# Kernel tuning notes

Hardware: AMD Instinct MI355X
Metric: run time of the kernel (lower is better)

Reference implementation:

```python
import jax, jax.numpy as jnp
import numpy as np

NUM_FEATURES = 1_000_000
EMB_DIM = 16
NUM_FIELDS = 39
CIN_SIZES = (200, 200, 200)
DNN_SIZES = (400, 400)


def setup_inputs() -> dict:
    key = jax.random.key(0)
    ks = jax.random.split(key, 16)
    B = 2048
    inp = {}
    inp["feature_ids"] = jax.random.randint(ks[0], (B, NUM_FIELDS), 0, NUM_FEATURES)
    inp["feature_vals"] = jax.random.uniform(ks[1], (B, NUM_FIELDS), dtype=jnp.float32)
    # embeddings (xavier-normal-ish scale)
    inp["emb"] = jax.random.normal(ks[2], (NUM_FEATURES, EMB_DIM), jnp.float32) * 0.02
    inp["bias_emb"] = jax.random.normal(ks[3], (NUM_FEATURES, 1), jnp.float32) * 0.02
    # CIN conv1d (kernel size 1) weights: (out, in)
    field_nums = [NUM_FIELDS]
    for i, size in enumerate(CIN_SIZES):
        cin_in = field_nums[-1] * NUM_FIELDS
        inp[f"cin_W{i}"] = jax.random.normal(ks[4 + i], (size, cin_in), jnp.float32) / np.sqrt(cin_in)
        inp[f"cin_b{i}"] = jnp.zeros((size,), jnp.float32)
        field_nums.append(size // 2 if i != len(CIN_SIZES) - 1 else size)
    # DNN linears: (out, in)
    last = NUM_FIELDS * EMB_DIM
    for i, size in enumerate(DNN_SIZES):
        inp[f"dnn_W{i}"] = jax.random.normal(ks[8 + i], (size, last), jnp.float32) / np.sqrt(last)
        inp[f"dnn_b{i}"] = jnp.zeros((size,), jnp.float32)
        last = size
    hidden_size = sum(CIN_SIZES[:-1]) // 2 + CIN_SIZES[-1]  # 400
    fc_in = hidden_size + DNN_SIZES[-1]
    inp["fc_W"] = jax.random.normal(ks[12], (1, fc_in), jnp.float32) / np.sqrt(fc_in)
    inp["fc_b"] = jnp.zeros((1,), jnp.float32)
    return inp


def _forward(feature_ids, feature_vals, emb, bias_emb,
             cin_W0, cin_b0, cin_W1, cin_b1, cin_W2, cin_b2,
             dnn_W0, dnn_b0, dnn_W1, dnn_b1, fc_W, fc_b):
    B = feature_ids.shape[0]
    inputs = emb[feature_ids] * feature_vals[:, :, None]        # [B, F, D]
    input_biases = bias_emb[feature_ids][..., 0] * feature_vals  # [B, F]

    # CIN
    Ws = (cin_W0, cin_W1, cin_W2)
    bs = (cin_b0, cin_b1, cin_b2)
    h = inputs
    finals = []
    n_layers = len(CIN_SIZES)
    for i in range(n_layers):
        size = CIN_SIZES[i]
        x = jnp.einsum('bhd,bmd->bhmd', h, inputs)              # [B, H, F, D]
        x = x.reshape(B, -1, EMB_DIM)                           # [B, H*F, D]
        x = jnp.einsum('bcd,oc->bod', x, Ws[i]) + bs[i][None, :, None]  # 1x1 conv
        x = jax.nn.relu(x)
        if i != n_layers - 1:
            h, direct = x[:, : size // 2], x[:, size // 2:]
        else:
            direct = x
        finals.append(direct)
    cin_result = jnp.sum(jnp.concatenate(finals, axis=1), axis=-1)  # [B, hidden]

    # DNN
    d = inputs.reshape(B, -1)
    d = jax.nn.relu(d @ dnn_W0.T + dnn_b0)
    d = jax.nn.relu(d @ dnn_W1.T + dnn_b1)

    out = (jnp.concatenate((cin_result, d), axis=1) @ fc_W.T + fc_b)[:, 0]
    return out + jnp.sum(input_biases, axis=1)                  # [B]


def reference(feature_ids, feature_vals, emb, bias_emb,
              cin_W0, cin_b0, cin_W1, cin_b1, cin_W2, cin_b2,
              dnn_W0, dnn_b0, dnn_W1, dnn_b1, fc_W, fc_b):
    return _forward(feature_ids, feature_vals, emb, bias_emb,
                    cin_W0, cin_b0, cin_W1, cin_b1, cin_W2, cin_b2,
                    dnn_W0, dnn_b0, dnn_W1, dnn_b1, fc_W, fc_b)
```

## Files before the change

kernel.cpp:

```cpp
#include <hip/hip_runtime.h>

#define B 2048
#define NF 39
#define D 16

typedef __bf16 bf16x8 __attribute__((ext_vector_type(8)));
typedef float f32x4 __attribute__((ext_vector_type(4)));

__global__ __launch_bounds__(256) void gather_kernel(
    const int* __restrict__ fid, const float* __restrict__ fval,
    const float* __restrict__ emb, const float* __restrict__ bias_emb,
    float* __restrict__ inputs, float* __restrict__ biassum) {
  int b = blockIdx.x;
  __shared__ int ids[NF];
  __shared__ float vals[NF];
  int t = threadIdx.x;
  if (t < NF) { ids[t] = fid[b * NF + t]; vals[t] = fval[b * NF + t]; }
  __syncthreads();
  for (int i = t; i < NF * D; i += 256) {
    int f = i >> 4, d = i & 15;
    inputs[b * NF * D + i] = emb[(long)ids[f] * D + d] * vals[f];
  }
  if (t < 64) {
    float pb = (t < NF) ? bias_emb[ids[t]] * vals[t] : 0.f;
#pragma unroll
    for (int m = 32; m >= 1; m >>= 1) pb += __shfl_xor(pb, m);
    if (t == 0) biassum[b] = pb;
  }
}

__global__ void prep_w_kernel(const float* __restrict__ W, __bf16* __restrict__ Wg,
                              int Hreal, int nch) {
  int idx = blockIdx.x * 256 + threadIdx.x;
  int total = nch * 13 * 64;
  if (idx >= total) return;
  int l = idx & 63;
  int mt = (idx >> 6) % 13;
  int c = idx / (13 * 64);
  int o = mt * 16 + (l & 15);
  int kb = c * 32 + ((l >> 4) << 3);
  int rowlen = Hreal * 39;
  bf16x8 v;
#pragma unroll
  for (int j = 0; j < 8; ++j) {
    int k = kb + j;
    int h = k / 40;
    int m = k - h * 40;
    float val = 0.f;
    if (o < 200 && h < Hreal && m < 39) val = W[(long)o * rowlen + h * 39 + m];
    v[j] = (__bf16)val;
  }
  *reinterpret_cast<bf16x8*>(Wg + (long)idx * 8) = v;
}

__global__ void prep_dnn_w(const float* __restrict__ W, __bf16* __restrict__ Wd,
                           int IN, int nch) {
  int idx = blockIdx.x * 256 + threadIdx.x;
  int total = nch * 25 * 64;
  if (idx >= total) return;
  int l = idx & 63;
  int tt = (idx >> 6) % 25;
  int c = idx / (25 * 64);
  int o = tt * 16 + (l & 15);
  int kb = c * 32 + ((l >> 4) << 3);
  bf16x8 v;
#pragma unroll
  for (int j = 0; j < 8; ++j) {
    int k = kb + j;
    v[j] = (k < IN) ? (__bf16)W[(long)o * IN + k] : (__bf16)0.f;
  }
  *reinterpret_cast<bf16x8*>(Wd + (long)idx * 8) = v;
}

__device__ __forceinline__ void form_x(const float* Hs, const float* Zs,
                                       __bf16* xbuf, int k0, int col) {
  int h = (int)((unsigned)k0 / 40u);
  int m0 = k0 - h * 40;
  float hv = Hs[h * 64 + col];
  const float4* zp = reinterpret_cast<const float4*>(Zs + col * 44 + m0);
  float4 za = zp[0], zb = zp[1];
  bf16x8 xv;
  xv[0] = (__bf16)(hv * za.x); xv[1] = (__bf16)(hv * za.y);
  xv[2] = (__bf16)(hv * za.z); xv[3] = (__bf16)(hv * za.w);
  xv[4] = (__bf16)(hv * zb.x); xv[5] = (__bf16)(hv * zb.y);
  xv[6] = (__bf16)(hv * zb.z); xv[7] = (__bf16)(hv * zb.w);
  int g = (k0 >> 3) & 7;
  *reinterpret_cast<bf16x8*>(
      reinterpret_cast<char*>(xbuf) + col * 128 + ((g * 16) ^ ((col & 7) << 4))) = xv;
}

template <int W, int NST, int SPLIT>
__device__ __forceinline__ void cin_core3(
    const float* Hs, const float* Zs, __bf16* Xs,
    const __bf16* __restrict__ Wg, const float* __restrict__ bias,
    float* __restrict__ h_next, float* __restrict__ cin_out,
    int col_offset, int bbase, int t) {
  constexpr int TLO = (13 * W) >> 2;
  const int l = t & 63;
  const int q = l >> 4;
  const int dd = l & 15;
  const int colw = t & 63;
  const __bf16* wl = Wg + l * 8;

  f32x4 acc[13] = {};
  bf16x8 wf[8], wfn[8];
#pragma unroll
  for (int i = 0; i < 4; ++i)
#pragma unroll
    for (int hf = 0; hf < 2; ++hf)
      wf[i * 2 + hf] =
          *reinterpret_cast<const bf16x8*>(wl + (long)((hf * 13 + TLO + i) * 64) * 8);

  form_x(Hs, Zs, Xs, (W) * 8, colw);
  form_x(Hs, Zs, Xs, (W + 4) * 8, colw);
  __syncthreads();

  for (int s = 0; s < NST; ++s) {
    __bf16* xcur = Xs + (s & 1) * (64 * 64);
    __bf16* xnxt = Xs + ((s + 1) & 1) * (64 * 64);
    if (s + 1 < NST) {
#pragma unroll
      for (int i = 0; i < 4; ++i)
#pragma unroll
        for (int hf = 0; hf < 2; ++hf)
          wfn[i * 2 + hf] = *reinterpret_cast<const bf16x8*>(
              wl + (long)((((s + 1) * 2 + hf) * 13 + TLO + i) * 64) * 8);
      form_x(Hs, Zs, xnxt, (s + 1) * 64 + W * 8, colw);
      form_x(Hs, Zs, xnxt, (s + 1) * 64 + (W + 4) * 8, colw);
    }
    bf16x8 bfr[4][2];
#pragma unroll
    for (int f = 0; f < 4; ++f)
#pragma unroll
      for (int hf = 0; hf < 2; ++hf) {
        int col = f * 16 + dd;
        int g = q + hf * 4;
        bfr[f][hf] = *reinterpret_cast<const bf16x8*>(
            reinterpret_cast<const char*>(xcur) + col * 128 +
            ((g * 16) ^ ((col & 7) << 4)));
      }
#pragma unroll
    for (int i = 0; i < 13; ++i) {
      const int p = 13 * W + i;
      const int ti = (p >> 2) - TLO;
      const int f = p & 3;
      acc[i] = __builtin_amdgcn_mfma_f32_16x16x32_bf16(wf[ti * 2 + 0], bfr[f][0],
                                                       acc[i], 0, 0, 0);
      acc[i] = __builtin_amdgcn_mfma_f32_16x16x32_bf16(wf[ti * 2 + 1], bfr[f][1],
                                                       acc[i], 0, 0, 0);
    }
    __syncthreads();
    if (s + 1 < NST) {
#pragma unroll
      for (int i = 0; i < 8; ++i) wf[i] = wfn[i];
    }
  }

#pragma unroll
  for (int i = 0; i < 13; ++i) {
    const int p = 13 * W + i;
    const int tt = p >> 2, f = p & 3;
    const int b = bbase + f;
#pragma unroll
    for (int r = 0; r < 4; ++r) {
      int o = tt * 16 + q * 4 + r;
      if (o < 200) {
        float x = fmaxf(acc[i][r] + bias[o], 0.f);
        if (SPLIT && o < 100) {
          h_next[((long)b * 100 + o) * 16 + dd] = x;
        } else {
          x += __shfl_xor(x, 1);
          x += __shfl_xor(x, 2);
          x += __shfl_xor(x, 4);
          x += __shfl_xor(x, 8);
          if (dd == 0) cin_out[b * 400 + col_offset + o - (SPLIT ? 100 : 0)] = x;
        }
      }
    }
  }
}

template <int HR, int NST, int SPLIT>
__global__ __launch_bounds__(256, 2) void cin_mfma3(
    const float* __restrict__ Zin, const float* __restrict__ Hin,
    const __bf16* __restrict__ Wg, const float* __restrict__ bias,
    float* __restrict__ h_next, float* __restrict__ cin_out, int col_offset) {
  constexpr int HPAD = (NST * 64 + 39) / 40;
  __shared__ float Hs[HPAD * 64];
  __shared__ float Zs[64 * 44];
  __shared__ __bf16 Xs[2 * 64 * 64];
  const int t = threadIdx.x;
  const int bbase = blockIdx.x * 4;

  for (int i = t; i < HPAD * 64; i += 256) {
    int h = i >> 6, col = i & 63;
    int b = bbase + (col >> 4), d = col & 15;
    Hs[i] = (h < HR) ? Hin[((long)b * HR + h) * 16 + d] : 0.f;
  }
  for (int i = t; i < 64 * 40; i += 256) {
    int col = i / 40, m = i - (i / 40) * 40;
    int b = bbase + (col >> 4), d = col & 15;
    Zs[col * 44 + m] = (m < NF) ? Zin[((long)b * NF + m) * 16 + d] : 0.f;
  }
  __syncthreads();

  const int w = t >> 6;
  if (w == 0)
    cin_core3<0, NST, SPLIT>(Hs, Zs, Xs, Wg, bias, h_next, cin_out, col_offset, bbase, t);
  else if (w == 1)
    cin_core3<1, NST, SPLIT>(Hs, Zs, Xs, Wg, bias, h_next, cin_out, col_offset, bbase, t);
  else if (w == 2)
    cin_core3<2, NST, SPLIT>(Hs, Zs, Xs, Wg, bias, h_next, cin_out, col_offset, bbase, t);
  else
    cin_core3<3, NST, SPLIT>(Hs, Zs, Xs, Wg, bias, h_next, cin_out, col_offset, bbase, t);
}

template <int IN>
__device__ __forceinline__ void dnn_stage(const float* __restrict__ x,
                                          __bf16* Xs, int bg, int c, int t) {
  int b = t >> 2, kb = t & 3;
  int k0 = c * 32 + kb * 8;
  bf16x8 v;
  if (k0 < IN) {
    const float4* p = reinterpret_cast<const float4*>(x + (long)(bg * 64 + b) * IN + k0);
    float4 a = p[0], bq = p[1];
    v[0] = (__bf16)a.x;  v[1] = (__bf16)a.y;  v[2] = (__bf16)a.z;  v[3] = (__bf16)a.w;
    v[4] = (__bf16)bq.x; v[5] = (__bf16)bq.y; v[6] = (__bf16)bq.z; v[7] = (__bf16)bq.w;
  } else {
#pragma unroll
    for (int j = 0; j < 8; ++j) v[j] = (__bf16)0.f;
  }
  *reinterpret_cast<bf16x8*>(Xs + ((kb * 64 + b) << 3)) = v;
}

template <int W, int MH, int IN, int NCH>
__device__ __forceinline__ void dnn_core(
    const float* __restrict__ x, const __bf16* __restrict__ Wd,
    const float* __restrict__ bias, float* __restrict__ out,
    __bf16* Xs, int bg, int t) {
  constexpr int NP = MH ? 12 : 13;
  constexpr int TLO = MH ? (13 + 3 * W) : ((13 * W) >> 2);
  constexpr int TN = MH ? 3 : 4;
  constexpr int WLO = MH ? (3 * W) : ((13 * W) >> 2);
  const int l = t & 63;
  const int q = l >> 4, dd = l & 15;
  const __bf16* wl = Wd + l * 8;

  f32x4 acc[NP] = {};
  bf16x8 wf[TN], wfn[TN];
#pragma unroll
  for (int i = 0; i < TN; ++i)
    wf[i] = *reinterpret_cast<const bf16x8*>(wl + (long)((TLO + i) * 64) * 8);

  dnn_stage<IN>(x, Xs, bg, 0, t);
  __syncthreads();

  for (int c = 0; c < NCH; ++c) {
    __bf16* cur = Xs + (c & 1) * 2048;
    __bf16* nxt = Xs + ((c + 1) & 1) * 2048;
    const bool more = (c + 1 < NCH);
    if (more) {
      dnn_stage<IN>(x, nxt, bg, c + 1, t);
#pragma unroll
      for (int i = 0; i < TN; ++i)
        wfn[i] = *reinterpret_cast<const bf16x8*>(
            wl + (long)(((c + 1) * 25 + TLO + i) * 64) * 8);
    }
    bf16x8 bfr[4];
#pragma unroll
    for (int f = 0; f < 4; ++f)
      bfr[f] = *reinterpret_cast<const bf16x8*>(cur + ((q * 64 + f * 16 + dd) << 3));
#pragma unroll
    for (int i = 0; i < NP; ++i) {
      const int p = NP * W + i;
      const int wfi = (p >> 2) - WLO;
      acc[i] = __builtin_amdgcn_mfma_f32_16x16x32_bf16(wf[wfi], bfr[p & 3], acc[i], 0, 0, 0);
    }
    __syncthreads();
    if (more) {
#pragma unroll
      for (int i = 0; i < TN; ++i) wf[i] = wfn[i];
    }
  }

#pragma unroll
  for (int i = 0; i < NP; ++i) {
    const int p = NP * W + i;
    const int gt = (MH ? 13 : 0) + (p >> 2);
    const int f = p & 3;
    const int b = bg * 64 + f * 16 + dd;
#pragma unroll
    for (int r = 0; r < 4; ++r) {
      int o = gt * 16 + q * 4 + r;
      out[(long)b * 400 + o] = fmaxf(acc[i][r] + bias[o], 0.f);
    }
  }
}

template <int IN, int NCH>
__global__ __launch_bounds__(256) void dnn_mfma(
    const float* __restrict__ x, const __bf16* __restrict__ Wd,
    const float* __restrict__ bias, float* __restrict__ out) {
  __shared__ __bf16 Xs[2 * 4 * 64 * 8];
  const int blk = blockIdx.x;
  const int bg = blk >> 1, mh = blk & 1;
  const int t = threadIdx.x;
  const int w = t >> 6;
  if (mh == 0) {
    if (w == 0) dnn_core<0, 0, IN, NCH>(x, Wd, bias, out, Xs, bg, t);
    else if (w == 1) dnn_core<1, 0, IN, NCH>(x, Wd, bias, out, Xs, bg, t);
    else if (w == 2) dnn_core<2, 0, IN, NCH>(x, Wd, bias, out, Xs, bg, t);
    else dnn_core<3, 0, IN, NCH>(x, Wd, bias, out, Xs, bg, t);
  } else {
    if (w == 0) dnn_core<0, 1, IN, NCH>(x, Wd, bias, out, Xs, bg, t);
    else if (w == 1) dnn_core<1, 1, IN, NCH>(x, Wd, bias, out, Xs, bg, t);
    else if (w == 2) dnn_core<2, 1, IN, NCH>(x, Wd, bias, out, Xs, bg, t);
    else dnn_core<3, 1, IN, NCH>(x, Wd, bias, out, Xs, bg, t);
  }
}

__global__ __launch_bounds__(256) void final_kernel(
    const float* __restrict__ cin, const float* __restrict__ d1,
    const float* __restrict__ fcW, const float* __restrict__ fcb,
    const float* __restrict__ biassum, float* __restrict__ out) {
  int b = blockIdx.x, t = threadIdx.x;
  float p = 0.f;
  for (int i = t; i < 800; i += 256) {
    float v = (i < 400) ? cin[b * 400 + i] : d1[b * 400 + (i - 400)];
    p += v * fcW[i];
  }
#pragma unroll
  for (int m = 32; m >= 1; m >>= 1) p += __shfl_xor(p, m);
  __shared__ float red[4];
  if ((t & 63) == 0) red[t >> 6] = p;
  __syncthreads();
  if (t == 0) out[b] = red[0] + red[1] + red[2] + red[3] + fcb[0] + biassum[b];
}

extern "C" void kernel_launch(void* const* d_in, const int* in_sizes, int n_in,
                              void* d_out, int out_size, void* d_ws,
                              size_t ws_size, hipStream_t stream) {
  (void)in_sizes; (void)n_in; (void)out_size; (void)ws_size;
  const int* fid = (const int*)d_in[0];
  const float* fval = (const float*)d_in[1];
  const float* emb = (const float*)d_in[2];
  const float* bias_emb = (const float*)d_in[3];
  const float* cW0 = (const float*)d_in[4];
  const float* cb0 = (const float*)d_in[5];
  const float* cW1 = (const float*)d_in[6];
  const float* cb1 = (const float*)d_in[7];
  const float* cW2 = (const float*)d_in[8];
  const float* cb2 = (const float*)d_in[9];
  const float* dW0 = (const float*)d_in[10];
  const float* db0 = (const float*)d_in[11];
  const float* dW1 = (const float*)d_in[12];
  const float* db1 = (const float*)d_in[13];
  const float* fcW = (const float*)d_in[14];
  const float* fcb = (const float*)d_in[15];
  float* out = (float*)d_out;

  float* ws = (float*)d_ws;
  float* inputs = ws;  ws += B * NF * D;
  float* biassum = ws; ws += B;
  float* h1 = ws;      ws += B * 100 * D;
  float* h2 = ws;      ws += B * 100 * D;
  float* cinres = ws;  ws += B * 400;
  float* dd0 = ws;     ws += B * 400;
  float* dd1 = ws;     ws += B * 400;
  __bf16* Wg0 = (__bf16*)ws; ws += (50 * 13 * 64 * 8) / 2;
  __bf16* Wg1 = (__bf16*)ws; ws += (126 * 13 * 64 * 8) / 2;
  __bf16* Wg2 = (__bf16*)ws; ws += (126 * 13 * 64 * 8) / 2;
  __bf16* Wd0 = (__bf16*)ws; ws += (20 * 25 * 64 * 8) / 2;
  __bf16* Wd1 = (__bf16*)ws; ws += (13 * 25 * 64 * 8) / 2;

  gather_kernel<<<B, 256, 0, stream>>>(fid, fval, emb, bias_emb, inputs, biassum);

  prep_w_kernel<<<(50 * 13 * 64 + 255) / 256, 256, 0, stream>>>(cW0, Wg0, 39, 50);
  prep_w_kernel<<<(126 * 13 * 64 + 255) / 256, 256, 0, stream>>>(cW1, Wg1, 100, 126);
  prep_w_kernel<<<(126 * 13 * 64 + 255) / 256, 256, 0, stream>>>(cW2, Wg2, 100, 126);
  prep_dnn_w<<<(20 * 25 * 64 + 255) / 256, 256, 0, stream>>>(dW0, Wd0, 624, 20);
  prep_dnn_w<<<(13 * 25 * 64 + 255) / 256, 256, 0, stream>>>(dW1, Wd1, 400, 13);

  cin_mfma3<39, 25, 1><<<B / 4, 256, 0, stream>>>(inputs, inputs, Wg0, cb0, h1, cinres, 0);
  cin_mfma3<100, 63, 1><<<B / 4, 256, 0, stream>>>(inputs, h1, Wg1, cb1, h2, cinres, 100);
  cin_mfma3<100, 63, 0><<<B / 4, 256, 0, stream>>>(inputs, h2, Wg2, cb2, nullptr, cinres, 200);

  dnn_mfma<624, 20><<<64, 256, 0, stream>>>(inputs, Wd0, db0, dd0);
  dnn_mfma<400, 13><<<64, 256, 0, stream>>>(dd0, Wd1, db1, dd1);

  final_kernel<<<B, 256, 0, stream>>>(cinres, dd1, fcW, fcb, biassum, out);
}
```

Baseline: 242.7 us.

## Fuse three CIN layers into one kernel and split DNN across more blocks

Merges the three CIN layer kernels into a single kernel that keeps the hidden state H in shared memory between layers. This removes the global round-trips for h1/h2 and two kernel launches. The DNN kernels now split output tiles four ways across 128 blocks instead of two ways across 64, and their staging loads are separated from the LDS writes so global latency overlaps the MFMAs. Both paths use s_setprio around the MFMA loops and a lighter LDS barrier; the fused CIN kernel's larger shared footprint and register use may reduce occupancy.

```diff
diff --git a/kernel.cpp b/kernel.cpp
--- a/kernel.cpp
+++ b/kernel.cpp
@@ -6,6 +6,11 @@
 
 typedef __bf16 bf16x8 __attribute__((ext_vector_type(8)));
 typedef float f32x4 __attribute__((ext_vector_type(4)));
+
+__device__ __forceinline__ void lds_barrier() {
+  asm volatile("s_waitcnt lgkmcnt(0)" ::: "memory");
+  __builtin_amdgcn_s_barrier();
+}
 
 __global__ __launch_bounds__(256) void gather_kernel(
     const int* __restrict__ fid, const float* __restrict__ fval,
@@ -89,44 +94,40 @@
       reinterpret_cast<char*>(xbuf) + col * 128 + ((g * 16) ^ ((col & 7) << 4))) = xv;
 }
 
-template <int W, int NST, int SPLIT>
-__device__ __forceinline__ void cin_core3(
-    const float* Hs, const float* Zs, __bf16* Xs,
+template <int NW, int NST, int SPLIT>
+__device__ __forceinline__ void cin_layer(
+    float* Hs, const float* Zs, __bf16* Xs,
     const __bf16* __restrict__ Wg, const float* __restrict__ bias,
-    float* __restrict__ h_next, float* __restrict__ cin_out,
-    int col_offset, int bbase, int t) {
-  constexpr int TLO = (13 * W) >> 2;
+    float* __restrict__ cin_out, int col_offset, int bbase, int t) {
+  constexpr int TLO = (13 * NW) >> 2;
   const int l = t & 63;
-  const int q = l >> 4;
-  const int dd = l & 15;
-  const int colw = t & 63;
-  const __bf16* wl = Wg + l * 8;
+  const int q = l >> 4, dd = l & 15;
 
   f32x4 acc[13] = {};
   bf16x8 wf[8], wfn[8];
+  const __bf16* wp = Wg + l * 8 + TLO * 512;
 #pragma unroll
   for (int i = 0; i < 4; ++i)
 #pragma unroll
     for (int hf = 0; hf < 2; ++hf)
-      wf[i * 2 + hf] =
-          *reinterpret_cast<const bf16x8*>(wl + (long)((hf * 13 + TLO + i) * 64) * 8);
-
-  form_x(Hs, Zs, Xs, (W) * 8, colw);
-  form_x(Hs, Zs, Xs, (W + 4) * 8, colw);
-  __syncthreads();
+      wf[i * 2 + hf] = *reinterpret_cast<const bf16x8*>(wp + hf * 6656 + i * 512);
+
+  form_x(Hs, Zs, Xs, NW * 8, l);
+  form_x(Hs, Zs, Xs, (NW + 4) * 8, l);
+  lds_barrier();
 
   for (int s = 0; s < NST; ++s) {
-    __bf16* xcur = Xs + (s & 1) * (64 * 64);
-    __bf16* xnxt = Xs + ((s + 1) & 1) * (64 * 64);
-    if (s + 1 < NST) {
+    __bf16* xcur = Xs + (s & 1) * 4096;
+    __bf16* xnxt = Xs + ((s + 1) & 1) * 4096;
+    const bool more = (s + 1 < NST);
+    if (more) {
+      const __bf16* wq = wp + 13312;
 #pragma unroll
       for (int i = 0; i < 4; ++i)
 #pragma unroll
         for (int hf = 0; hf < 2; ++hf)
-          wfn[i * 2 + hf] = *reinterpret_cast<const bf16x8*>(
-              wl + (long)((((s + 1) * 2 + hf) * 13 + TLO + i) * 64) * 8);
-      form_x(Hs, Zs, xnxt, (s + 1) * 64 + W * 8, colw);
-      form_x(Hs, Zs, xnxt, (s + 1) * 64 + (W + 4) * 8, colw);
+          wfn[i * 2 + hf] =
+              *reinterpret_cast<const bf16x8*>(wq + hf * 6656 + i * 512);
     }
     bf16x8 bfr[4][2];
 #pragma unroll
@@ -139,9 +140,14 @@
             reinterpret_cast<const char*>(xcur) + col * 128 +
             ((g * 16) ^ ((col & 7) << 4)));
       }
+    if (more) {
+      form_x(Hs, Zs, xnxt, (s + 1) * 64 + NW * 8, l);
+      form_x(Hs, Zs, xnxt, (s + 1) * 64 + (NW + 4) * 8, l);
+    }
+    __builtin_amdgcn_s_setprio(1);
 #pragma unroll
     for (int i = 0; i < 13; ++i) {
-      const int p = 13 * W + i;
+      const int p = 13 * NW + i;
       const int ti = (p >> 2) - TLO;
       const int f = p & 3;
       acc[i] = __builtin_amdgcn_mfma_f32_16x16x32_bf16(wf[ti * 2 + 0], bfr[f][0],
@@ -149,16 +155,18 @@
       acc[i] = __builtin_amdgcn_mfma_f32_16x16x32_bf16(wf[ti * 2 + 1], bfr[f][1],
                                                        acc[i], 0, 0, 0);
     }
-    __syncthreads();
-    if (s + 1 < NST) {
+    __builtin_amdgcn_s_setprio(0);
+    lds_barrier();
+    if (more) {
 #pragma unroll
       for (int i = 0; i < 8; ++i) wf[i] = wfn[i];
+      wp += 13312;
     }
   }
 
 #pragma unroll
   for (int i = 0; i < 13; ++i) {
-    const int p = 13 * W + i;
+    const int p = 13 * NW + i;
     const int tt = p >> 2, f = p & 3;
     const int b = bbase + f;
 #pragma unroll
@@ -167,7 +175,7 @@
       if (o < 200) {
         float x = fmaxf(acc[i][r] + bias[o], 0.f);
         if (SPLIT && o < 100) {
-          h_next[((long)b * 100 + o) * 16 + dd] = x;
+          Hs[o * 64 + f * 16 + dd] = x;
         } else {
           x += __shfl_xor(x, 1);
           x += __shfl_xor(x, 2);
@@ -178,105 +186,126 @@
       }
     }
   }
-}
-
-template <int HR, int NST, int SPLIT>
-__global__ __launch_bounds__(256, 2) void cin_mfma3(
-    const float* __restrict__ Zin, const float* __restrict__ Hin,
-    const __bf16* __restrict__ Wg, const float* __restrict__ bias,
-    float* __restrict__ h_next, float* __restrict__ cin_out, int col_offset) {
-  constexpr int HPAD = (NST * 64 + 39) / 40;
-  __shared__ float Hs[HPAD * 64];
+  lds_barrier();
+}
+
+template <int NW>
+__device__ __forceinline__ void cin_all(
+    float* Hs, const float* Zs, __bf16* Xs, const __bf16* Wg0,
+    const __bf16* Wg1, const __bf16* Wg2, const float* cb0, const float* cb1,
+    const float* cb2, float* cinres, int bbase, int t) {
+  cin_layer<NW, 25, 1>(Hs, Zs, Xs, Wg0, cb0, cinres, 0, bbase, t);
+  cin_layer<NW, 63, 1>(Hs, Zs, Xs, Wg1, cb1, cinres, 100, bbase, t);
+  cin_layer<NW, 63, 0>(Hs, Zs, Xs, Wg2, cb2, cinres, 200, bbase, t);
+}
+
+__global__ __launch_bounds__(256, 2) void cin_fused(
+    const float* __restrict__ Zin, const __bf16* __restrict__ Wg0,
+    const __bf16* __restrict__ Wg1, const __bf16* __restrict__ Wg2,
+    const float* __restrict__ cb0, const float* __restrict__ cb1,
+    const float* __restrict__ cb2, float* __restrict__ cinres) {
+  __shared__ float Hs[101 * 64];
   __shared__ float Zs[64 * 44];
   __shared__ __bf16 Xs[2 * 64 * 64];
   const int t = threadIdx.x;
   const int bbase = blockIdx.x * 4;
 
-  for (int i = t; i < HPAD * 64; i += 256) {
-    int h = i >> 6, col = i & 63;
-    int b = bbase + (col >> 4), d = col & 15;
-    Hs[i] = (h < HR) ? Hin[((long)b * HR + h) * 16 + d] : 0.f;
-  }
   for (int i = t; i < 64 * 40; i += 256) {
     int col = i / 40, m = i - (i / 40) * 40;
     int b = bbase + (col >> 4), d = col & 15;
     Zs[col * 44 + m] = (m < NF) ? Zin[((long)b * NF + m) * 16 + d] : 0.f;
   }
+  for (int i = t; i < 41 * 64; i += 256) {
+    int h = i >> 6, col = i & 63;
+    int b = bbase + (col >> 4), d = col & 15;
+    Hs[i] = (h < NF) ? Zin[((long)b * NF + h) * 16 + d] : 0.f;
+  }
+  if (t < 64) Hs[100 * 64 + t] = 0.f;
   __syncthreads();
 
   const int w = t >> 6;
-  if (w == 0)
-    cin_core3<0, NST, SPLIT>(Hs, Zs, Xs, Wg, bias, h_next, cin_out, col_offset, bbase, t);
-  else if (w == 1)
-    cin_core3<1, NST, SPLIT>(Hs, Zs, Xs, Wg, bias, h_next, cin_out, col_offset, bbase, t);
-  else if (w == 2)
-    cin_core3<2, NST, SPLIT>(Hs, Zs, Xs, Wg, bias, h_next, cin_out, col_offset, bbase, t);
-  else
-    cin_core3<3, NST, SPLIT>(Hs, Zs, Xs, Wg, bias, h_next, cin_out, col_offset, bbase, t);
+  if (w == 0) cin_all<0>(Hs, Zs, Xs, Wg0, Wg1, Wg2, cb0, cb1, cb2, cinres, bbase, t);
+  else if (w == 1) cin_all<1>(Hs, Zs, Xs, Wg0, Wg1, Wg2, cb0, cb1, cb2, cinres, bbase, t);
+  else if (w == 2) cin_all<2>(Hs, Zs, Xs, Wg0, Wg1, Wg2, cb0, cb1, cb2, cinres, bbase, t);
+  else cin_all<3>(Hs, Zs, Xs, Wg0, Wg1, Wg2, cb0, cb1, cb2, cinres, bbase, t);
 }
 
 template <int IN>
-__device__ __forceinline__ void dnn_stage(const float* __restrict__ x,
-                                          __bf16* Xs, int bg, int c, int t) {
+__device__ __forceinline__ void dnn_stage_load(const float* __restrict__ x,
+                                               int bg, int c, int t,
+                                               float4& a, float4& b2) {
   int b = t >> 2, kb = t & 3;
   int k0 = c * 32 + kb * 8;
+  if (k0 < IN) {
+    const float4* p =
+        reinterpret_cast<const float4*>(x + (long)(bg * 64 + b) * IN + k0);
+    a = p[0];
+    b2 = p[1];
+  } else {
+    a = make_float4(0.f, 0.f, 0.f, 0.f);
+    b2 = make_float4(0.f, 0.f, 0.f, 0.f);
+  }
+}
+
+__device__ __forceinline__ void dnn_stage_write(__bf16* Xs, int t, float4 a,
+                                                float4 b2) {
+  int b = t >> 2, kb = t & 3;
   bf16x8 v;
-  if (k0 < IN) {
-    const float4* p = reinterpret_cast<const float4*>(x + (long)(bg * 64 + b) * IN + k0);
-    float4 a = p[0], bq = p[1];
-    v[0] = (__bf16)a.x;  v[1] = (__bf16)a.y;  v[2] = (__bf16)a.z;  v[3] = (__bf16)a.w;
-    v[4] = (__bf16)bq.x; v[5] = (__bf16)bq.y; v[6] = (__bf16)bq.z; v[7] = (__bf16)bq.w;
-  } else {
-#pragma unroll
-    for (int j = 0; j < 8; ++j) v[j] = (__bf16)0.f;
-  }
+  v[0] = (__bf16)a.x;  v[1] = (__bf16)a.y;  v[2] = (__bf16)a.z;  v[3] = (__bf16)a.w;
+  v[4] = (__bf16)b2.x; v[5] = (__bf16)b2.y; v[6] = (__bf16)b2.z; v[7] = (__bf16)b2.w;
   *reinterpret_cast<bf16x8*>(Xs + ((kb * 64 + b) << 3)) = v;
 }
 
-template <int W, int MH, int IN, int NCH>
+template <int W, int TG, int IN, int NCH>
 __device__ __forceinline__ void dnn_core(
     const float* __restrict__ x, const __bf16* __restrict__ Wd,
-    const float* __restrict__ bias, float* __restrict__ out,
-    __bf16* Xs, int bg, int t) {
-  constexpr int NP = MH ? 12 : 13;
-  constexpr int TLO = MH ? (13 + 3 * W) : ((13 * W) >> 2);
-  constexpr int TN = MH ? 3 : 4;
-  constexpr int WLO = MH ? (3 * W) : ((13 * W) >> 2);
+    const float* __restrict__ bias, float* __restrict__ out, __bf16* Xs,
+    int bg, int t) {
+  constexpr int NT = (TG == 3) ? 7 : 6;
+  constexpr int TGB = TG * 6;
+  constexpr int PLO = NT * W;
+  constexpr int TLO = PLO >> 2;
+  constexpr int TN = ((PLO + NT - 1) >> 2) - TLO + 1;
   const int l = t & 63;
   const int q = l >> 4, dd = l & 15;
   const __bf16* wl = Wd + l * 8;
 
-  f32x4 acc[NP] = {};
+  f32x4 acc[NT] = {};
   bf16x8 wf[TN], wfn[TN];
 #pragma unroll
   for (int i = 0; i < TN; ++i)
-    wf[i] = *reinterpret_cast<const bf16x8*>(wl + (long)((TLO + i) * 64) * 8);
-
-  dnn_stage<IN>(x, Xs, bg, 0, t);
-  __syncthreads();
+    wf[i] = *reinterpret_cast<const bf16x8*>(wl + (long)((TGB + TLO + i) * 64) * 8);
+
+  float4 ra, rb;
+  dnn_stage_load<IN>(x, bg, 0, t, ra, rb);
+  dnn_stage_write(Xs, t, ra, rb);
+  lds_barrier();
 
   for (int c = 0; c < NCH; ++c) {
     __bf16* cur = Xs + (c & 1) * 2048;
     __bf16* nxt = Xs + ((c + 1) & 1) * 2048;
     const bool more = (c + 1 < NCH);
     if (more) {
-      dnn_stage<IN>(x, nxt, bg, c + 1, t);
+      dnn_stage_load<IN>(x, bg, c + 1, t, ra, rb);
 #pragma unroll
       for (int i = 0; i < TN; ++i)
         wfn[i] = *reinterpret_cast<const bf16x8*>(
-            wl + (long)(((c + 1) * 25 + TLO + i) * 64) * 8);
+            wl + (long)(((c + 1) * 25 + TGB + TLO + i) * 64) * 8);
     }
     bf16x8 bfr[4];
 #pragma unroll
     for (int f = 0; f < 4; ++f)
       bfr[f] = *reinterpret_cast<const bf16x8*>(cur + ((q * 64 + f * 16 + dd) << 3));
-#pragma unroll
-    for (int i = 0; i < NP; ++i) {
-      const int p = NP * W + i;
-      const int wfi = (p >> 2) - WLO;
-      acc[i] = __builtin_amdgcn_mfma_f32_16x16x32_bf16(wf[wfi], bfr[p & 3], acc[i], 0, 0, 0);
-    }
-    __syncthreads();
+    __builtin_amdgcn_s_setprio(1);
+#pragma unroll
+    for (int i = 0; i < NT; ++i) {
+      const int p = PLO + i;
+      acc[i] = __builtin_amdgcn_mfma_f32_16x16x32_bf16(wf[(p >> 2) - TLO],
+                                                       bfr[p & 3], acc[i], 0, 0, 0);
+    }
+    __builtin_amdgcn_s_setprio(0);
+    if (more) dnn_stage_write(nxt, t, ra, rb);
+    lds_barrier();
     if (more) {
 #pragma unroll
       for (int i = 0; i < TN; ++i) wf[i] = wfn[i];
@@ -284,9 +313,9 @@
   }
 
 #pragma unroll
-  for (int i = 0; i < NP; ++i) {
-    const int p = NP * W + i;
-    const int gt = (MH ? 13 : 0) + (p >> 2);
+  for (int i = 0; i < NT; ++i) {
+    const int p = PLO + i;
+    const int gt = TGB + (p >> 2);
     const int f = p & 3;
     const int b = bg * 64 + f * 16 + dd;
 #pragma unroll
@@ -303,20 +332,19 @@
     const float* __restrict__ bias, float* __restrict__ out) {
   __shared__ __bf16 Xs[2 * 4 * 64 * 8];
   const int blk = blockIdx.x;
-  const int bg = blk >> 1, mh = blk & 1;
+  const int bg = blk >> 2, tg = blk & 3;
   const int t = threadIdx.x;
   const int w = t >> 6;
-  if (mh == 0) {
-    if (w == 0) dnn_core<0, 0, IN, NCH>(x, Wd, bias, out, Xs, bg, t);
-    else if (w == 1) dnn_core<1, 0, IN, NCH>(x, Wd, bias, out, Xs, bg, t);
-    else if (w == 2) dnn_core<2, 0, IN, NCH>(x, Wd, bias, out, Xs, bg, t);
-    else dnn_core<3, 0, IN, NCH>(x, Wd, bias, out, Xs, bg, t);
-  } else {
-    if (w == 0) dnn_core<0, 1, IN, NCH>(x, Wd, bias, out, Xs, bg, t);
-    else if (w == 1) dnn_core<1, 1, IN, NCH>(x, Wd, bias, out, Xs, bg, t);
-    else if (w == 2) dnn_core<2, 1, IN, NCH>(x, Wd, bias, out, Xs, bg, t);
-    else dnn_core<3, 1, IN, NCH>(x, Wd, bias, out, Xs, bg, t);
-  }
+#define DNN_DISPATCH(TGV)                                                     \
+  if (w == 0) dnn_core<0, TGV, IN, NCH>(x, Wd, bias, out, Xs, bg, t);         \
+  else if (w == 1) dnn_core<1, TGV, IN, NCH>(x, Wd, bias, out, Xs, bg, t);    \
+  else if (w == 2) dnn_core<2, TGV, IN, NCH>(x, Wd, bias, out, Xs, bg, t);    \
+  else dnn_core<3, TGV, IN, NCH>(x, Wd, bias, out, Xs, bg, t);
+  if (tg == 0) { DNN_DISPATCH(0) }
+  else if (tg == 1) { DNN_DISPATCH(1) }
+  else if (tg == 2) { DNN_DISPATCH(2) }
+  else { DNN_DISPATCH(3) }
+#undef DNN_DISPATCH
 }
 
 __global__ __launch_bounds__(256) void final_kernel(
@@ -362,8 +390,6 @@
   float* ws = (float*)d_ws;
   float* inputs = ws;  ws += B * NF * D;
   float* biassum = ws; ws += B;
-  float* h1 = ws;      ws += B * 100 * D;
-  float* h2 = ws;      ws += B * 100 * D;
   float* cinres = ws;  ws += B * 400;
   float* dd0 = ws;     ws += B * 400;
   float* dd1 = ws;     ws += B * 400;
@@ -381,12 +407,10 @@
   prep_dnn_w<<<(20 * 25 * 64 + 255) / 256, 256, 0, stream>>>(dW0, Wd0, 624, 20);
   prep_dnn_w<<<(13 * 25 * 64 + 255) / 256, 256, 0, stream>>>(dW1, Wd1, 400, 13);
 
-  cin_mfma3<39, 25, 1><<<B / 4, 256, 0, stream>>>(inputs, inputs, Wg0, cb0, h1, cinres, 0);
-  cin_mfma3<100, 63, 1><<<B / 4, 256, 0, stream>>>(inputs, h1, Wg1, cb1, h2, cinres, 100);
-  cin_mfma3<100, 63, 0><<<B / 4, 256, 0, stream>>>(inputs, h2, Wg2, cb2, nullptr, cinres, 200);
-
-  dnn_mfma<624, 20><<<64, 256, 0, stream>>>(inputs, Wd0, db0, dd0);
-  dnn_mfma<400, 13><<<64, 256, 0, stream>>>(dd0, Wd1, db1, dd1);
+  cin_fused<<<B / 4, 256, 0, stream>>>(inputs, Wg0, Wg1, Wg2, cb0, cb1, cb2, cinres);
+
+  dnn_mfma<624, 20><<<128, 256, 0, stream>>>(inputs, Wd0, db0, dd0);
+  dnn_mfma<400, 13><<<128, 256, 0, stream>>>(dd0, Wd1, db1, dd1);
 
   final_kernel<<<B, 256, 0, stream>>>(cinres, dd1, fcW, fcb, biassum, out);
 }
```

After: 212.7 us. 12.4% less time.
